# Kernel optimization log

Hardware: AMD Instinct MI355X
Metric: run time of the kernel (lower is better)

## Reference

```python
import jax, jax.numpy as jnp
import numpy as np

B, IN_DIM, D, H, L = 16, 4096, 100, 200, 4
N, E = B * IN_DIM, 8 * B * IN_DIM
EPS = 1e-7  # GENConv message eps


def setup_inputs() -> dict:
    key = jax.random.key(0)
    ks = jax.random.split(key, 16)
    s = 0.05
    return {
        "x": jax.random.normal(ks[0], (N, 1), jnp.float32),
        "edge_index": jax.random.randint(ks[1], (2, E), 0, N),
        "batch_ids": jnp.repeat(jnp.arange(B), IN_DIM),  # graphs of exactly IN_DIM nodes
        "enc_w": jax.random.normal(ks[2], (1, D), jnp.float32) * s,
        "enc_b": jnp.zeros((D,), jnp.float32),
        "h1_w": jax.random.normal(ks[3], (IN_DIM, 1000), jnp.float32) * 0.02,
        "h1_b": jnp.zeros((1000,), jnp.float32),
        "h2_w": jax.random.normal(ks[4], (1000, 100), jnp.float32) * s,
        "h2_b": jnp.zeros((100,), jnp.float32),
        "ln_g": jnp.ones((L, D), jnp.float32),
        "ln_b": jnp.zeros((L, D), jnp.float32),
        "w1": jax.random.normal(ks[5], (L, D, H), jnp.float32) * s,
        "b1": jnp.zeros((L, H), jnp.float32),
        "bn_g": jnp.ones((L, H), jnp.float32),
        "bn_b": jnp.zeros((L, H), jnp.float32),
        "w2": jax.random.normal(ks[6], (L, H, D), jnp.float32) * s,
        "b2": jnp.zeros((L, D), jnp.float32),
        "dec_w": jax.random.normal(ks[7], (D, 1), jnp.float32) * s,
        "dec_b": jnp.zeros((1,), jnp.float32),
    }


def reference(x, edge_index, batch_ids, enc_w, enc_b, h1_w, h1_b, h2_w, h2_b,
              ln_g, ln_b, w1, b1, bn_g, bn_b, w2, b2, dec_w, dec_b):
    src, dst = edge_index[0], edge_index[1]
    # dense branch: [B, IN_DIM] -> 1000 -> 100 with leaky_relu (dropout p=0)
    xs = x.reshape(B, IN_DIM)
    xs = jax.nn.leaky_relu(xs @ h1_w + h1_b, 0.01)
    xs = jax.nn.leaky_relu(xs @ h2_w + h2_b, 0.01)

    h = x @ enc_w + enc_b  # node encoder -> [N, D]
    for i in range(L):  # DeepGCNLayer res+: x + GENConv(dropout(relu(LN(x))))
        mu = jnp.mean(h, axis=-1, keepdims=True)
        var = jnp.mean((h - mu) ** 2, axis=-1, keepdims=True)
        hn = (h - mu) * jax.lax.rsqrt(var + 1e-5) * ln_g[i] + ln_b[i]
        hn = jnp.maximum(hn, 0.0)  # act (dropout in eval mode = identity)
        # GENConv: message = relu(x_j) + eps, softmax aggregation (t=1)
        m = jnp.maximum(hn[src], 0.0) + EPS            # [E, D]
        mx = jax.ops.segment_max(m, dst, num_segments=N)
        ex = jnp.exp(m - mx[dst])
        den = jax.ops.segment_sum(ex, dst, num_segments=N)
        agg = jax.ops.segment_sum((ex / den[dst]) * m, dst, num_segments=N)
        # out = mlp(agg + x): Linear(D,2D) -> BN(eval) -> ReLU -> Linear(2D,D)
        z = (agg + hn) @ w1[i] + b1[i]
        z = jnp.maximum(z * bn_g[i] + bn_b[i], 0.0)
        h = h + (z @ w2[i] + b2[i])

    pooled = jax.ops.segment_sum(h, batch_ids, num_segments=B) / IN_DIM
    out = 0.5 * xs + 0.5 * pooled
    return (out @ dec_w + dec_b)[:, 0]
```

## Files before the change

### kernel.cpp

```cpp
#include <hip/hip_runtime.h>
#include <hip/hip_bf16.h>
#include <hip/hip_fp16.h>
#include <math.h>

#define B_ 16
#define IN_DIM_ 4096
#define D_ 100
#define H_ 200
#define L_ 4
#define N_ (B_*IN_DIM_)
#define E_ (8*B_*IN_DIM_)
#define EPS_ 1e-7f

typedef __attribute__((ext_vector_type(8))) short bf16x8s;
typedef __attribute__((ext_vector_type(4))) float f32x4;

__device__ inline unsigned pack_bf16x2(float a, float b){
  __hip_bfloat16 x = __float2bfloat16(a), y = __float2bfloat16(b);
  unsigned short ux = *(unsigned short*)&x, uy = *(unsigned short*)&y;
  return (unsigned)ux | ((unsigned)uy << 16);
}
__device__ inline __half2 u2h(unsigned v){ return *(__half2*)&v; }

__device__ inline unsigned char f2fp8(float v){
  unsigned p = __builtin_amdgcn_cvt_pk_fp8_f32(v, 0.f, 0u, false);
  return (unsigned char)(p & 0xFF);
}

#define ENC_BLKS_ 16384
#define DEG_BLKS_ 2048
#define D1_BLKS_  256
#define PREP_BLKS_ 448
#define SETUP_BLKS_ (ENC_BLKS_+DEG_BLKS_+D1_BLKS_+PREP_BLKS_)

__global__ void setup_kernel(const float* __restrict__ x, const float* __restrict__ enc_w,
                             const float* __restrict__ enc_b, const float* __restrict__ g0,
                             const float* __restrict__ b0,
                             __half* __restrict__ h, char* __restrict__ hnb,
                             char* __restrict__ hnb8,
                             const int* __restrict__ dsts, int* __restrict__ deg,
                             const float* __restrict__ h1_w, float* __restrict__ xs1acc,
                             const float* __restrict__ w1, const float* __restrict__ w2,
                             __hip_bfloat16* __restrict__ w1T, __hip_bfloat16* __restrict__ w2T) {
  __shared__ float xl[16][64];
  int bid = blockIdx.x;
  int t = threadIdx.x;
  if (bid < ENC_BLKS_) {
    int wid = (bid*256 + t) >> 6;
    int lane = t & 63;
    float xn = x[wid];
    int c0 = 2*lane, c1 = c0+1;
    bool v = c0 < D_;
    float h0=0.f, h1=0.f;
    if (v){ h0 = fmaf(xn, enc_w[c0], enc_b[c0]); h1 = fmaf(xn, enc_w[c1], enc_b[c1]); }
    float s = h0+h1;
    #pragma unroll
    for (int off=32; off; off>>=1) s += __shfl_xor(s, off, 64);
    float mu = s * (1.f/D_);
    float d0 = v? h0-mu : 0.f, d1 = v? h1-mu : 0.f;
    float q = d0*d0 + d1*d1;
    #pragma unroll
    for (int off=32; off; off>>=1) q += __shfl_xor(q, off, 64);
    float rstd = rsqrtf(q*(1.f/D_) + 1e-5f);
    if (c0 < 112) *(__half2*)&h[(size_t)wid*112 + c0] = __floats2half2_rn(h0, h1);
    float n0 = v? fmaxf(fmaf(d0*rstd, g0[c0], b0[c0]), 0.f) : 0.f;
    float n1 = v? fmaxf(fmaf(d1*rstd, g0[c1], b0[c1]), 0.f) : 0.f;
    *(__half2*)(hnb + (size_t)wid*256 + 4*lane) = __floats2half2_rn(n0, n1);
    unsigned short p8 = (unsigned short)f2fp8(n0) | ((unsigned short)f2fp8(n1) << 8);
    *(unsigned short*)(hnb8 + (size_t)wid*128 + c0) = p8;
  } else if (bid < ENC_BLKS_+DEG_BLKS_) {
    int e = (bid-ENC_BLKS_)*256 + t;
    if (e < E_) atomicAdd(&deg[dsts[e]], 1);
  } else if (bid < ENC_BLKS_+DEG_BLKS_+D1_BLKS_) {
    int l = bid - (ENC_BLKS_+DEG_BLKS_);
    int bx = l & 3, by = l >> 2;
    int k0 = by * 64;
    for (int i = t; i < 16*64; i += 256) {
      int b = i >> 6, kk = i & 63;
      xl[b][kk] = x[b*IN_DIM_ + k0 + kk];
    }
    __syncthreads();
    int c = bx*256 + t;
    if (c >= 1000) return;
    float acc[B_];
    #pragma unroll
    for (int b=0;b<B_;b++) acc[b]=0.f;
    #pragma unroll 4
    for (int kk=0; kk<64; kk++) {
      float w = h1_w[(k0+kk)*1000 + c];
      #pragma unroll
      for (int b=0;b<B_;b++) acc[b] += xl[b][kk]*w;
    }
    #pragma unroll
    for (int b=0;b<B_;b++) atomicAdd(&xs1acc[b*1000+c], acc[b]);
  } else {
    int idx = (bid - (ENC_BLKS_+DEG_BLKS_+D1_BLKS_))*256 + t;
    if (idx < L_*224*128) {
      int l = idx / (224*128);
      int rem = idx % (224*128);
      int col = rem / 128, k = rem % 128;
      float v = (col < H_ && k < D_) ? w1[(l*D_ + k)*H_ + col] : 0.f;
      w1T[idx] = __float2bfloat16(v);
    }
    if (idx < L_*112*224) {
      int l = idx / (112*224);
      int rem = idx % (112*224);
      int col = rem / 224, k = rem % 224;
      float v = (col < D_ && k < H_) ? w2[(l*H_ + k)*D_ + col] : 0.f;
      w2T[idx] = __float2bfloat16(v);
    }
  }
}

__global__ void stage2_kernel(const int* __restrict__ deg, int* __restrict__ row_start,
                              const float* __restrict__ xs1acc, const float* __restrict__ h1_b,
                              const float* __restrict__ h2_w, float* __restrict__ xs2acc) {
  __shared__ int sums[1024];
  int t = threadIdx.x;
  if (blockIdx.x == 0) {
    int base = t*64;
    int s = 0;
    for (int j=0;j<64;j++) s += deg[base+j];
    sums[t] = s;
    __syncthreads();
    for (int off=1; off<1024; off<<=1){
      int add = (t>=off)? sums[t-off] : 0;
      __syncthreads();
      sums[t] += add;
      __syncthreads();
    }
    int excl = (t==0)? 0 : sums[t-1];
    int run = excl;
    for (int j=0;j<64;j++){ row_start[base+j] = run; run += deg[base+j]; }
    if (t==1023) row_start[N_] = run;
  } else {
    int T = (blockIdx.x-1)*1024 + t;
    if (T >= 100*40) return;
    int c = T % 100, kc = T / 100;
    int k0 = kc*25;
    float acc[B_];
    #pragma unroll
    for (int b=0;b<B_;b++) acc[b]=0.f;
    for (int kk=0;kk<25;kk++){
      int k = k0+kk;
      float w = h2_w[k*100 + c];
      float bk = h1_b[k];
      #pragma unroll
      for (int b=0;b<B_;b++){
        float m = xs1acc[b*1000+k] + bk;
        m = (m>0.f)? m : 0.01f*m;
        acc[b] += m*w;
      }
    }
    #pragma unroll
    for (int b=0;b<B_;b++) atomicAdd(&xs2acc[b*100+c], acc[b]);
  }
}

__global__ void scatter_kernel(const int* __restrict__ srcs, const int* __restrict__ dst,
                               const int* __restrict__ row_start, int* __restrict__ cnt,
                               int* __restrict__ sorted_src) {
  int e = blockIdx.x*256+threadIdx.x;
  if (e < E_){
    int d = dst[e];
    int p = row_start[d] + atomicAdd(&cnt[d], 1);
    sorted_src[p] = srcs[e];
  }
}

__global__ void agg_kernel(const char* __restrict__ hnb, const char* __restrict__ hnb8,
                           const int* __restrict__ row_start,
                           const int* __restrict__ sorted_src, unsigned* __restrict__ u) {
  int gw = (blockIdx.x*256 + threadIdx.x) >> 6;
  int lane = threadIdx.x & 63;
  int lpos = lane & 31;
  int gbase = lane & 32;
  int node = gw*2 + (lane >> 5);
  int beg = row_start[node];
  int deg = row_start[node+1] - beg;
  int mdeg = deg;
  #pragma unroll
  for (int m=1; m<64; m<<=1) { int o = __shfl_xor(mdeg, m, 64); mdeg = mdeg > o ? mdeg : o; }
  const char* lanep8 = hnb8 + 4*lpos;
  float s0=0.f,s1=0.f,s2=0.f,s3=0.f, w0=0.f,w1=0.f,w2=0.f,w3=0.f;

#define CONSUME_(R) { \
    float v0=__builtin_amdgcn_cvt_f32_fp8(R,0)+EPS_; \
    float v1=__builtin_amdgcn_cvt_f32_fp8(R,1)+EPS_; \
    float v2=__builtin_amdgcn_cvt_f32_fp8(R,2)+EPS_; \
    float v3=__builtin_amdgcn_cvt_f32_fp8(R,3)+EPS_; \
    float e0=__expf(v0), e1=__expf(v1), e2=__expf(v2), e3=__expf(v3); \
    s0+=e0; w0=fmaf(e0,v0,w0); s1+=e1; w1=fmaf(e1,v1,w1); \
    s2+=e2; w2=fmaf(e2,v2,w2); s3+=e3; w3=fmaf(e3,v3,w3); }

  for (int cb=0; cb<mdeg; cb+=32){
    int cidx = (cb + lpos < deg) ? sorted_src[beg + cb + lpos] : 0;
    int cnt = mdeg - cb; if (cnt > 32) cnt = 32;
    int grem = deg - cb;
    int glim = grem < cnt ? grem : cnt; if (glim < 0) glim = 0;
    unsigned r0=0, r1=0, r2=0, r3=0;
    if (0 < glim) r0 = *(const unsigned*)(lanep8 + (size_t)__shfl(cidx, gbase+0)*128);
    if (1 < glim) r1 = *(const unsigned*)(lanep8 + (size_t)__shfl(cidx, gbase+1)*128);
    if (2 < glim) r2 = *(const unsigned*)(lanep8 + (size_t)__shfl(cidx, gbase+2)*128);
    if (3 < glim) r3 = *(const unsigned*)(lanep8 + (size_t)__shfl(cidx, gbase+3)*128);
    for (int j=0; j<cnt; j+=4){
      unsigned n0=0, n1=0, n2=0, n3=0;
      if (j+4 < glim) n0 = *(const unsigned*)(lanep8 + (size_t)__shfl(cidx, gbase+j+4)*128);
      if (j+5 < glim) n1 = *(const unsigned*)(lanep8 + (size_t)__shfl(cidx, gbase+j+5)*128);
      if (j+6 < glim) n2 = *(const unsigned*)(lanep8 + (size_t)__shfl(cidx, gbase+j+6)*128);
      if (j+7 < glim) n3 = *(const unsigned*)(lanep8 + (size_t)__shfl(cidx, gbase+j+7)*128);
      if (j   < glim) CONSUME_(r0);
      if (j+1 < glim) CONSUME_(r1);
      if (j+2 < glim) CONSUME_(r2);
      if (j+3 < glim) CONSUME_(r3);
      r0=n0; r1=n1; r2=n2; r3=n3;
    }
  }
#undef CONSUME_

  uint2 own = *(const uint2*)(hnb + (size_t)node*256 + 8*lpos);
  __half2 oa = u2h(own.x), ob = u2h(own.y);
  float u0 = ((deg>0)? w0/s0 : 0.f) + __low2float(oa);
  float u1 = ((deg>0)? w1/s1 : 0.f) + __high2float(oa);
  float u2 = ((deg>0)? w2/s2 : 0.f) + __low2float(ob);
  float u3 = ((deg>0)? w3/s3 : 0.f) + __high2float(ob);
  if (lpos >= 25) { u0=0.f; u1=0.f; u2=0.f; u3=0.f; }
  uint2 outv; outv.x = pack_bf16x2(u0,u1); outv.y = pack_bf16x2(u2,u3);
  *(uint2*)((char*)u + (size_t)node*256 + 8*lpos) = outv;
}

__global__ __launch_bounds__(256,4) void gemm1_kernel(
    const char* __restrict__ u, const __hip_bfloat16* __restrict__ w1T,
    const float* __restrict__ b1, const float* __restrict__ bng, const float* __restrict__ bnb,
    char* __restrict__ z) {
  __shared__ __align__(16) char wL[112*272];
  int bid = blockIdx.x;
  int half = bid & 1;
  size_t row0 = (size_t)(bid >> 1) * 64;
  int t = threadIdx.x;
  const char* wg = (const char*)w1T + (size_t)half*112*256;
  #pragma unroll
  for (int c = t; c < 1792; c += 256) {
    int r = c >> 4, sb = (c & 15) << 4;
    *(float4*)(wL + r*272 + sb) = *(const float4*)(wg + (size_t)r*256 + sb);
  }
  __syncthreads();
  int wave = t >> 6, lane = t & 63;
  int l15 = lane & 15;
  int kgb = (lane >> 4) << 4;
  int ar = wave*16 + l15;
  bf16x8s a[4];
  #pragma unroll
  for (int ks=0; ks<4; ks++)
    a[ks] = *(const bf16x8s*)(u + (row0 + ar)*256 + ks*64 + kgb);
  f32x4 acc[7];
  #pragma unroll
  for (int n=0;n<7;n++) acc[n] = (f32x4){0.f,0.f,0.f,0.f};
  #pragma unroll
  for (int ks=0; ks<4; ks++) {
    int kb = ks*64 + kgb;
    #pragma unroll
    for (int n=0;n<7;n++) {
      bf16x8s b = *(const bf16x8s*)(wL + (n*16 + l15)*272 + kb);
      acc[n] = __builtin_amdgcn_mfma_f32_16x16x32_bf16(a[ks], b, acc[n], 0, 0, 0);
    }
  }
  size_t rbase = row0 + wave*16 + ((lane>>4)<<2);
  #pragma unroll
  for (int n=0;n<7;n++) {
    int col = half*112 + n*16 + l15;
    float bias = (col < H_) ? b1[col] : 0.f;
    float g    = (col < H_) ? bng[col] : 0.f;
    float bb   = (col < H_) ? bnb[col] : 0.f;
    #pragma unroll
    for (int r=0;r<4;r++) {
      float v = fmaxf((acc[n][r] + bias)*g + bb, 0.f);
      if (col >= H_) v = 0.f;
      *(__hip_bfloat16*)(z + (rbase + r)*448 + 2*col) = __float2bfloat16(v);
    }
  }
}

template<int LAST>
__global__ __launch_bounds__(256,3) void gemm2_kernel(
    const char* __restrict__ z, const __hip_bfloat16* __restrict__ w2T,
    const float* __restrict__ b2, __half* __restrict__ h,
    const float* __restrict__ lng, const float* __restrict__ lnb,
    char* __restrict__ hnb, char* __restrict__ hnb8, float* __restrict__ pooled) {
  __shared__ __align__(16) char wL[112*464];
  int t = threadIdx.x;
  size_t row0 = (size_t)blockIdx.x * 64;
  const char* wg = (const char*)w2T;
  for (int c = t; c < 3136; c += 256) {
    int r = c / 28, sb = (c - r*28) << 4;
    *(float4*)(wL + r*464 + sb) = *(const float4*)(wg + (size_t)r*448 + sb);
  }
  __syncthreads();
  int wave = t >> 6, lane = t & 63;
  int l15 = lane & 15;
  int kgb = (lane >> 4) << 4;
  int ar = wave*16 + l15;
  bf16x8s a[7];
  #pragma unroll
  for (int ks=0; ks<7; ks++)
    a[ks] = *(const bf16x8s*)(z + (row0 + ar)*448 + ks*64 + kgb);
  f32x4 acc[7];
  #pragma unroll
  for (int n=0;n<7;n++) acc[n] = (f32x4){0.f,0.f,0.f,0.f};
  #pragma unroll
  for (int ks=0; ks<7; ks++) {
    int kb = ks*64 + kgb;
    #pragma unroll
    for (int n=0;n<7;n++) {
      bf16x8s b = *(const bf16x8s*)(wL + (n*16 + l15)*464 + kb);
      acc[n] = __builtin_amdgcn_mfma_f32_16x16x32_bf16(a[ks], b, acc[n], 0, 0, 0);
    }
  }
  size_t rbase = row0 + wave*16 + ((lane>>4)<<2);

  float x_[7][4];
  float sum[4]  = {0,0,0,0};
  float sum2[4] = {0,0,0,0};
  float psum[7] = {0,0,0,0,0,0,0};
  #pragma unroll
  for (int n=0;n<7;n++) {
    int col = n*16 + l15;
    bool valid = col < D_;
    float bias = valid ? b2[col] : 0.f;
    #pragma unroll
    for (int r=0;r<4;r++) {
      float xv = 0.f;
      if (valid) xv = acc[n][r] + bias + __half2float(h[(rbase + r)*112 + col]);
      x_[n][r] = xv;
      if (LAST) {
        psum[n] += xv;
      } else {
        sum[r] += xv; sum2[r] += xv*xv;
        if (valid) h[(rbase + r)*112 + col] = __float2half(xv);
      }
    }
  }

  if (LAST) {
    #pragma unroll
    for (int n=0;n<7;n++) {
      psum[n] += __shfl_xor(psum[n], 16, 64);
      psum[n] += __shfl_xor(psum[n], 32, 64);
    }
    __syncthreads();
    float* ps = (float*)wL;
    if (lane < 16) {
      #pragma unroll
      for (int n=0;n<7;n++) ps[wave*112 + n*16 + l15] = psum[n];
    }
    __syncthreads();
    if (t < D_) {
      float v = ps[t] + ps[112+t] + ps[224+t] + ps[336+t];
      int b = (int)(row0 >> 12);
      atomicAdd(&pooled[b*D_ + t], v);
    }
  } else {
    #pragma unroll
    for (int r=0;r<4;r++) {
      float s = sum[r], s2 = sum2[r];
      #pragma unroll
      for (int m=1;m<16;m<<=1) { s += __shfl_xor(s, m, 16); s2 += __shfl_xor(s2, m, 16); }
      sum[r] = s; sum2[r] = s2;
    }
    #pragma unroll
    for (int n=0;n<7;n++) {
      int col = n*16 + l15;
      float g  = (col < D_) ? lng[col] : 0.f;
      float be = (col < D_) ? lnb[col] : 0.f;
      #pragma unroll
      for (int r=0;r<4;r++) {
        float mu = sum[r]*(1.f/D_);
        float var = sum2[r]*(1.f/D_) - mu*mu;
        float rstd = rsqrtf(var + 1e-5f);
        float hv = fmaxf(fmaf((x_[n][r]-mu)*rstd, g, be), 0.f);
        if (col >= D_) hv = 0.f;
        *(__half*)(hnb + (rbase + r)*256 + 2*col) = __float2half(hv);
        *(unsigned char*)(hnb8 + (rbase + r)*128 + col) = f2fp8(hv);
      }
    }
    {
      int col = 112 + l15;
      __half zh = __float2half(0.f);
      #pragma unroll
      for (int r=0;r<4;r++) {
        *(__half*)(hnb + (rbase + r)*256 + 2*col) = zh;
        *(unsigned char*)(hnb8 + (rbase + r)*128 + col) = 0;
      }
    }
  }
}

__global__ void final_kernel(const float* __restrict__ xs2acc, const float* __restrict__ h2_b,
                             const float* __restrict__ pooled,
                             const float* __restrict__ dec_w, const float* __restrict__ dec_b,
                             float* __restrict__ out) {
  __shared__ float red[128];
  int t = threadIdx.x;
  for (int b=0;b<B_;b++){
    float v = 0.f;
    if (t < D_) {
      float xs = xs2acc[b*D_+t] + h2_b[t];
      xs = (xs>0.f)? xs : 0.01f*xs;
      v = (0.5f*xs + (0.5f/IN_DIM_)*pooled[b*D_+t]) * dec_w[t];
    }
    red[t] = v;
    __syncthreads();
    for (int off=64; off; off>>=1){
      if (t < off) red[t] += red[t+off];
      __syncthreads();
    }
    if (t==0) out[b] = red[0] + dec_b[0];
    __syncthreads();
  }
}

extern "C" void kernel_launch(void* const* d_in, const int* in_sizes, int n_in,
                              void* d_out, int out_size, void* d_ws, size_t ws_size,
                              hipStream_t stream) {
  const float* x      = (const float*)d_in[0];
  const int*   eidx   = (const int*)d_in[1];
  const float* enc_w  = (const float*)d_in[3];
  const float* enc_b  = (const float*)d_in[4];
  const float* h1_w   = (const float*)d_in[5];
  const float* h1_b   = (const float*)d_in[6];
  const float* h2_w   = (const float*)d_in[7];
  const float* h2_b   = (const float*)d_in[8];
  const float* ln_g   = (const float*)d_in[9];
  const float* ln_b   = (const float*)d_in[10];
  const float* w1     = (const float*)d_in[11];
  const float* b1     = (const float*)d_in[12];
  const float* bn_g   = (const float*)d_in[13];
  const float* bn_b   = (const float*)d_in[14];
  const float* w2     = (const float*)d_in[15];
  const float* b2     = (const float*)d_in[16];
  const float* dec_w  = (const float*)d_in[17];
  const float* dec_b  = (const float*)d_in[18];
  float* out = (float*)d_out;

  char* ws = (char*)d_ws;
  size_t off = 0;
  auto alloc = [&](size_t bytes)->char* {
    char* p = ws + off;
    off += (bytes + 255) & ~(size_t)255;
    return p;
  };
  __half* h     = (__half*)alloc((size_t)N_*112*2);
  char*  hnb    = alloc((size_t)N_*256);
  char*  hnb8   = alloc((size_t)N_*128);
  char*  z      = alloc((size_t)N_*448);
  unsigned* u   = (unsigned*)alloc((size_t)N_*64*4);
  __hip_bfloat16* w1T = (__hip_bfloat16*)alloc((size_t)L_*224*128*2);
  __hip_bfloat16* w2T = (__hip_bfloat16*)alloc((size_t)L_*112*224*2);
  char* zb = alloc(16*1000*4 + 16*100*4 + 16*100*4 + N_*4 + N_*4);
  float* xs1    = (float*)zb;
  float* xs2    = (float*)(zb + 64000);
  float* pooled = (float*)(zb + 64000 + 6400);
  int* deg      = (int*)(zb + 64000 + 6400 + 6400);
  int* cnt      = (int*)(zb + 64000 + 6400 + 6400 + N_*4);
  int* row_start  = (int*)alloc((N_+1)*4);
  int* sorted_src = (int*)alloc(E_*4);

  const int* srcs = eidx;
  const int* dsts = eidx + E_;

  hipMemsetAsync(zb, 0, 64000 + 6400 + 6400 + (size_t)N_*4*2, stream);

  setup_kernel<<<SETUP_BLKS_, 256, 0, stream>>>(x, enc_w, enc_b, ln_g, ln_b, h, hnb, hnb8,
                                                dsts, deg, h1_w, xs1, w1, w2, w1T, w2T);
  stage2_kernel<<<5, 1024, 0, stream>>>(deg, row_start, xs1, h1_b, h2_w, xs2);
  scatter_kernel<<<E_/256, 256, 0, stream>>>(srcs, dsts, row_start, cnt, sorted_src);

  for (int i=0;i<L_;i++){
    agg_kernel<<<N_/8, 256, 0, stream>>>(hnb, hnb8, row_start, sorted_src, u);
    gemm1_kernel<<<(N_/64)*2, 256, 0, stream>>>((const char*)u,
                                                w1T + (size_t)i*224*128, b1 + i*H_,
                                                bn_g + i*H_, bn_b + i*H_, z);
    if (i < L_-1) {
      gemm2_kernel<0><<<N_/64, 256, 0, stream>>>(z, w2T + (size_t)i*112*224, b2 + i*D_,
                                                 h, ln_g + (i+1)*D_, ln_b + (i+1)*D_,
                                                 hnb, hnb8, pooled);
    } else {
      gemm2_kernel<1><<<N_/64, 256, 0, stream>>>(z, w2T + (size_t)i*112*224, b2 + i*D_,
                                                 h, nullptr, nullptr, hnb, hnb8, pooled);
    }
  }

  final_kernel<<<1, 128, 0, stream>>>(xs2, h2_b, pooled, dec_w, dec_b, out);
}
```

Measured before the change: 422.9 us.

## Bucket nodes by in-degree so each aggregation wave handles similar-degree nodes

Builds a degree histogram, scans it into bin offsets and writes a node permutation `order` sorted by in-degree, which agg_kernel now uses to pick its nodes. Each 64-lane wave loops up to the larger in-degree of its two nodes, so grouping similar degrees is meant to cut idle lanes and loop iterations. In exchange it adds an extra kernel launch, more work in the stage2 and scatter kernels, and an indirection that scatters the per-node output writes. Separately, setup_kernel now runs the dense first-layer GEMV first, with 64 larger blocks over 256-wide K chunks instead of 256 blocks, which cuts the number of atomic adds.

After: 414.7 us. No clear change (-1.9%).

```diff
diff --git a/kernel.cpp b/kernel.cpp
--- a/kernel.cpp
+++ b/kernel.cpp
@@ -27,11 +27,11 @@
   return (unsigned char)(p & 0xFF);
 }
 
+#define D1_BLKS_  64
+#define PREP_BLKS_ 448
+#define DEG_BLKS_ 2048
 #define ENC_BLKS_ 16384
-#define DEG_BLKS_ 2048
-#define D1_BLKS_  256
-#define PREP_BLKS_ 448
-#define SETUP_BLKS_ (ENC_BLKS_+DEG_BLKS_+D1_BLKS_+PREP_BLKS_)
+#define SETUP_BLKS_ (D1_BLKS_+PREP_BLKS_+DEG_BLKS_+ENC_BLKS_)
 
 __global__ void setup_kernel(const float* __restrict__ x, const float* __restrict__ enc_w,
                              const float* __restrict__ enc_b, const float* __restrict__ g0,
@@ -42,11 +42,51 @@
                              const float* __restrict__ h1_w, float* __restrict__ xs1acc,
                              const float* __restrict__ w1, const float* __restrict__ w2,
                              __hip_bfloat16* __restrict__ w1T, __hip_bfloat16* __restrict__ w2T) {
-  __shared__ float xl[16][64];
+  __shared__ float xl[16][256];
   int bid = blockIdx.x;
   int t = threadIdx.x;
-  if (bid < ENC_BLKS_) {
-    int wid = (bid*256 + t) >> 6;
+  if (bid < D1_BLKS_) {
+    int bx = bid & 3, by = bid >> 2;
+    int k0 = by * 256;
+    for (int i = t; i < 16*256; i += 256) {
+      int b = i >> 8, kk = i & 255;
+      xl[b][kk] = x[b*IN_DIM_ + k0 + kk];
+    }
+    __syncthreads();
+    int c = bx*256 + t;
+    if (c >= 1000) return;
+    float acc[B_];
+    #pragma unroll
+    for (int b=0;b<B_;b++) acc[b]=0.f;
+    #pragma unroll 4
+    for (int kk=0; kk<256; kk++) {
+      float w = h1_w[(size_t)(k0+kk)*1000 + c];
+      #pragma unroll
+      for (int b=0;b<B_;b++) acc[b] += xl[b][kk]*w;
+    }
+    #pragma unroll
+    for (int b=0;b<B_;b++) atomicAdd(&xs1acc[b*1000+c], acc[b]);
+  } else if (bid < D1_BLKS_+PREP_BLKS_) {
+    int idx = (bid - D1_BLKS_)*256 + t;
+    if (idx < L_*224*128) {
+      int l = idx / (224*128);
+      int rem = idx % (224*128);
+      int col = rem / 128, k = rem % 128;
+      float v = (col < H_ && k < D_) ? w1[(l*D_ + k)*H_ + col] : 0.f;
+      w1T[idx] = __float2bfloat16(v);
+    }
+    if (idx < L_*112*224) {
+      int l = idx / (112*224);
+      int rem = idx % (112*224);
+      int col = rem / 224, k = rem % 224;
+      float v = (col < D_ && k < H_) ? w2[(l*H_ + k)*D_ + col] : 0.f;
+      w2T[idx] = __float2bfloat16(v);
+    }
+  } else if (bid < D1_BLKS_+PREP_BLKS_+DEG_BLKS_) {
+    int e = (bid - (D1_BLKS_+PREP_BLKS_))*256 + t;
+    if (e < E_) atomicAdd(&deg[dsts[e]], 1);
+  } else {
+    int wid = ((bid - (D1_BLKS_+PREP_BLKS_+DEG_BLKS_))*256 + t) >> 6;
     int lane = t & 63;
     float xn = x[wid];
     int c0 = 2*lane, c1 = c0+1;
@@ -68,56 +108,17 @@
     *(__half2*)(hnb + (size_t)wid*256 + 4*lane) = __floats2half2_rn(n0, n1);
     unsigned short p8 = (unsigned short)f2fp8(n0) | ((unsigned short)f2fp8(n1) << 8);
     *(unsigned short*)(hnb8 + (size_t)wid*128 + c0) = p8;
-  } else if (bid < ENC_BLKS_+DEG_BLKS_) {
-    int e = (bid-ENC_BLKS_)*256 + t;
-    if (e < E_) atomicAdd(&deg[dsts[e]], 1);
-  } else if (bid < ENC_BLKS_+DEG_BLKS_+D1_BLKS_) {
-    int l = bid - (ENC_BLKS_+DEG_BLKS_);
-    int bx = l & 3, by = l >> 2;
-    int k0 = by * 64;
-    for (int i = t; i < 16*64; i += 256) {
-      int b = i >> 6, kk = i & 63;
-      xl[b][kk] = x[b*IN_DIM_ + k0 + kk];
-    }
-    __syncthreads();
-    int c = bx*256 + t;
-    if (c >= 1000) return;
-    float acc[B_];
-    #pragma unroll
-    for (int b=0;b<B_;b++) acc[b]=0.f;
-    #pragma unroll 4
-    for (int kk=0; kk<64; kk++) {
-      float w = h1_w[(k0+kk)*1000 + c];
-      #pragma unroll
-      for (int b=0;b<B_;b++) acc[b] += xl[b][kk]*w;
-    }
-    #pragma unroll
-    for (int b=0;b<B_;b++) atomicAdd(&xs1acc[b*1000+c], acc[b]);
-  } else {
-    int idx = (bid - (ENC_BLKS_+DEG_BLKS_+D1_BLKS_))*256 + t;
-    if (idx < L_*224*128) {
-      int l = idx / (224*128);
-      int rem = idx % (224*128);
-      int col = rem / 128, k = rem % 128;
-      float v = (col < H_ && k < D_) ? w1[(l*D_ + k)*H_ + col] : 0.f;
-      w1T[idx] = __float2bfloat16(v);
-    }
-    if (idx < L_*112*224) {
-      int l = idx / (112*224);
-      int rem = idx % (112*224);
-      int col = rem / 224, k = rem % 224;
-      float v = (col < D_ && k < H_) ? w2[(l*H_ + k)*D_ + col] : 0.f;
-      w2T[idx] = __float2bfloat16(v);
-    }
   }
 }
 
 __global__ void stage2_kernel(const int* __restrict__ deg, int* __restrict__ row_start,
                               const float* __restrict__ xs1acc, const float* __restrict__ h1_b,
-                              const float* __restrict__ h2_w, float* __restrict__ xs2acc) {
+                              const float* __restrict__ h2_w, float* __restrict__ xs2acc,
+                              int* __restrict__ hist) {
   __shared__ int sums[1024];
   int t = threadIdx.x;
-  if (blockIdx.x == 0) {
+  int bid = blockIdx.x;
+  if (bid == 0) {
     int base = t*64;
     int s = 0;
     for (int j=0;j<64;j++) s += deg[base+j];
@@ -133,8 +134,8 @@
     int run = excl;
     for (int j=0;j<64;j++){ row_start[base+j] = run; run += deg[base+j]; }
     if (t==1023) row_start[N_] = run;
-  } else {
-    int T = (blockIdx.x-1)*1024 + t;
+  } else if (bid <= 4) {
+    int T = (bid-1)*1024 + t;
     if (T >= 100*40) return;
     int c = T % 100, kc = T / 100;
     int k0 = kc*25;
@@ -154,28 +155,72 @@
     }
     #pragma unroll
     for (int b=0;b<B_;b++) atomicAdd(&xs2acc[b*100+c], acc[b]);
-  }
+  } else {
+    __shared__ int lh[256];
+    if (t < 256) lh[t] = 0;
+    __syncthreads();
+    int base = (bid-5)*16384;
+    for (int n = base + t; n < base + 16384; n += 1024) {
+      int d = deg[n]; if (d > 255) d = 255;
+      atomicAdd(&lh[d], 1);
+    }
+    __syncthreads();
+    if (t < 256 && lh[t] > 0) atomicAdd(&hist[t], lh[t]);
+  }
+}
+
+__global__ void binscan_kernel(const int* __restrict__ hist, int* __restrict__ binoff,
+                               int* __restrict__ bincnt) {
+  __shared__ int s[256];
+  int t = threadIdx.x;
+  int hv = hist[t];
+  s[t] = hv;
+  __syncthreads();
+  for (int off=1; off<256; off<<=1){
+    int v = (t>=off)? s[t-off] : 0;
+    __syncthreads();
+    s[t] += v;
+    __syncthreads();
+  }
+  binoff[t] = s[t] - hv;
+  bincnt[t] = 0;
 }
 
 __global__ void scatter_kernel(const int* __restrict__ srcs, const int* __restrict__ dst,
                                const int* __restrict__ row_start, int* __restrict__ cnt,
-                               int* __restrict__ sorted_src) {
-  int e = blockIdx.x*256+threadIdx.x;
-  if (e < E_){
+                               int* __restrict__ sorted_src,
+                               const int* __restrict__ deg, const int* __restrict__ binoff,
+                               int* __restrict__ bincnt, int* __restrict__ order) {
+  int bid = blockIdx.x;
+  int t = threadIdx.x;
+  if (bid < 2048) {
+    int e = bid*256 + t;
     int d = dst[e];
     int p = row_start[d] + atomicAdd(&cnt[d], 1);
     sorted_src[p] = srcs[e];
+  } else {
+    __shared__ int lh[256], lbase[256];
+    int n = (bid-2048)*256 + t;
+    int d = deg[n]; int b = (d > 255) ? 255 : d;
+    lh[t] = 0;
+    __syncthreads();
+    int myrank = atomicAdd(&lh[b], 1);
+    __syncthreads();
+    lbase[t] = (lh[t] > 0) ? atomicAdd(&bincnt[t], lh[t]) : 0;
+    __syncthreads();
+    order[binoff[b] + lbase[b] + myrank] = n;
   }
 }
 
 __global__ void agg_kernel(const char* __restrict__ hnb, const char* __restrict__ hnb8,
                            const int* __restrict__ row_start,
-                           const int* __restrict__ sorted_src, unsigned* __restrict__ u) {
+                           const int* __restrict__ sorted_src,
+                           const int* __restrict__ order, unsigned* __restrict__ u) {
   int gw = (blockIdx.x*256 + threadIdx.x) >> 6;
   int lane = threadIdx.x & 63;
   int lpos = lane & 31;
   int gbase = lane & 32;
-  int node = gw*2 + (lane >> 5);
+  int node = order[gw*2 + (lane >> 5)];
   int beg = row_start[node];
   int deg = row_start[node+1] - beg;
   int mdeg = deg;
@@ -456,27 +501,34 @@
   unsigned* u   = (unsigned*)alloc((size_t)N_*64*4);
   __hip_bfloat16* w1T = (__hip_bfloat16*)alloc((size_t)L_*224*128*2);
   __hip_bfloat16* w2T = (__hip_bfloat16*)alloc((size_t)L_*112*224*2);
-  char* zb = alloc(16*1000*4 + 16*100*4 + 16*100*4 + N_*4 + N_*4);
+  size_t zbsz = 64000 + 6400 + 6400 + (size_t)N_*4 + (size_t)N_*4 + 1024;
+  char* zb = alloc(zbsz);
   float* xs1    = (float*)zb;
   float* xs2    = (float*)(zb + 64000);
   float* pooled = (float*)(zb + 64000 + 6400);
   int* deg      = (int*)(zb + 64000 + 6400 + 6400);
-  int* cnt      = (int*)(zb + 64000 + 6400 + 6400 + N_*4);
+  int* cnt      = (int*)(zb + 64000 + 6400 + 6400 + (size_t)N_*4);
+  int* hist     = (int*)(zb + 64000 + 6400 + 6400 + (size_t)N_*8);
   int* row_start  = (int*)alloc((N_+1)*4);
-  int* sorted_src = (int*)alloc(E_*4);
+  int* sorted_src = (int*)alloc((size_t)E_*4);
+  int* order      = (int*)alloc((size_t)N_*4);
+  int* binoff     = (int*)alloc(1024);
+  int* bincnt     = (int*)alloc(1024);
 
   const int* srcs = eidx;
   const int* dsts = eidx + E_;
 
-  hipMemsetAsync(zb, 0, 64000 + 6400 + 6400 + (size_t)N_*4*2, stream);
+  hipMemsetAsync(zb, 0, zbsz, stream);
 
   setup_kernel<<<SETUP_BLKS_, 256, 0, stream>>>(x, enc_w, enc_b, ln_g, ln_b, h, hnb, hnb8,
                                                 dsts, deg, h1_w, xs1, w1, w2, w1T, w2T);
-  stage2_kernel<<<5, 1024, 0, stream>>>(deg, row_start, xs1, h1_b, h2_w, xs2);
-  scatter_kernel<<<E_/256, 256, 0, stream>>>(srcs, dsts, row_start, cnt, sorted_src);
+  stage2_kernel<<<9, 1024, 0, stream>>>(deg, row_start, xs1, h1_b, h2_w, xs2, hist);
+  binscan_kernel<<<1, 256, 0, stream>>>(hist, binoff, bincnt);
+  scatter_kernel<<<2048+256, 256, 0, stream>>>(srcs, dsts, row_start, cnt, sorted_src,
+                                               deg, binoff, bincnt, order);
 
   for (int i=0;i<L_;i++){
-    agg_kernel<<<N_/8, 256, 0, stream>>>(hnb, hnb8, row_start, sorted_src, u);
+    agg_kernel<<<N_/8, 256, 0, stream>>>(hnb, hnb8, row_start, sorted_src, order, u);
     gemm1_kernel<<<(N_/64)*2, 256, 0, stream>>>((const char*)u,
                                                 w1T + (size_t)i*224*128, b1 + i*H_,
                                                 bn_g + i*H_, bn_b + i*H_, z);
```
